# Kernel tuning notes

Measured on AMD Instinct MI355X. Metric: run time of the kernel, lower is better.

Reference implementation:

```python
import jax, jax.numpy as jnp
import numpy as np
import math

B, N, C, H = 8, 1024, 768, 12
D = C // H
HID = 4 * C
LS_INIT = 1e-6
LN_EPS = 1e-5


def setup_inputs() -> dict:
    key = jax.random.key(0)
    ks = jax.random.split(key, 8)
    s = lambda fan: 1.0 / math.sqrt(fan)
    return {
        'x': jax.random.normal(ks[0], (B, N, C), jnp.float32),
        'ln1_w': jnp.ones((C,), jnp.float32),
        'ln1_b': jnp.zeros((C,), jnp.float32),
        'qkv_w': jax.random.uniform(ks[1], (3 * C, C), jnp.float32, -s(C), s(C)),
        'qkv_b': jnp.zeros((3 * C,), jnp.float32),
        'proj_w': jax.random.uniform(ks[2], (C, C), jnp.float32, -s(C), s(C)),
        'proj_b': jnp.zeros((C,), jnp.float32),
        'attn_bias': jnp.asarray(-math.log(N), jnp.float32),
        'ls1': jnp.full((C,), LS_INIT, jnp.float32),
        'ln2_w': jnp.ones((C,), jnp.float32),
        'ln2_b': jnp.zeros((C,), jnp.float32),
        'w1': jax.random.uniform(ks[3], (HID, C), jnp.float32, -s(C), s(C)),
        'b1': jnp.zeros((HID,), jnp.float32),
        'w2': jax.random.uniform(ks[4], (C, HID), jnp.float32, -s(HID), s(HID)),
        'b2': jnp.zeros((C,), jnp.float32),
        'ls2': jnp.full((C,), LS_INIT, jnp.float32),
    }


def _layernorm(x, w, b):
    mu = jnp.mean(x, axis=-1, keepdims=True)
    var = jnp.mean(jnp.square(x - mu), axis=-1, keepdims=True)
    return (x - mu) * jax.lax.rsqrt(var + LN_EPS) * w + b


def reference(x, ln1_w, ln1_b, qkv_w, qkv_b, proj_w, proj_b, attn_bias,
              ls1, ln2_w, ln2_b, w1, b1, w2, b2, ls2):
    # --- sigmoid attention branch ---
    h = _layernorm(x, ln1_w, ln1_b)                       # [B,N,C]
    qkv = h @ qkv_w.T + qkv_b                              # [B,N,3C]
    qkv = qkv.reshape(B, N, 3, H, D).transpose(2, 0, 3, 1, 4)
    q, k, v = qkv[0], qkv[1], qkv[2]                       # [B,H,N,D]
    scale = D ** -0.5
    scores = jnp.einsum('bhnd,bhmd->bhnm', q, k) * scale + attn_bias
    attn = jax.nn.sigmoid(scores)                          # [B,H,N,N]
    o = jnp.einsum('bhnm,bhmd->bhnd', attn, v)             # [B,H,N,D]
    o = o.transpose(0, 2, 1, 3).reshape(B, N, C)
    o = o @ proj_w.T + proj_b
    x = x + o * ls1
    # --- MLP branch ---
    h2 = _layernorm(x, ln2_w, ln2_b)
    m = jax.nn.gelu(h2 @ w1.T + b1, approximate=False)
    m = m @ w2.T + b2
    x = x + m * ls2
    return x
```

## Files before the change

### kernel.cpp

```cpp
#include <hip/hip_runtime.h>
#include <math.h>

static constexpr int Bv   = 8;
static constexpr int Nv   = 1024;
static constexpr int Cv   = 768;
static constexpr int Hv   = 12;
static constexpr int HIDv = 3072;
static constexpr int Mv   = Bv * Nv;

typedef __attribute__((ext_vector_type(4)))  float f32x4;
typedef __attribute__((ext_vector_type(16))) float f32x16;
typedef __attribute__((ext_vector_type(8)))  short s16x8;
typedef __attribute__((ext_vector_type(4)))  short s16x4;

__device__ __forceinline__ short f2bf(float f) {
  union { float f; unsigned u; } c; c.f = f;
  unsigned r = c.u + 0x7fffu + ((c.u >> 16) & 1u);
  return (short)(r >> 16);
}

__device__ __forceinline__ void gload16(const void* g, void* l) {
  __builtin_amdgcn_global_load_lds(
      (const __attribute__((address_space(1))) unsigned*)g,
      (__attribute__((address_space(3))) unsigned*)l, 16, 0, 0);
}

__device__ __forceinline__ unsigned ldsaddr(const void* p) {
  return (unsigned)(size_t)(const __attribute__((address_space(3))) char*)p;
}

__device__ __forceinline__ float fsigmoid_exp2(float t) {
  return __builtin_amdgcn_rcpf(1.0f + __builtin_amdgcn_exp2f(t));
}

__global__ __launch_bounds__(256) void cvt_kernel(const float* __restrict__ in,
                                                  short* __restrict__ out, int n4) {
  int i = blockIdx.x * 256 + threadIdx.x;
  if (i >= n4) return;
  float4 v = ((const float4*)in)[i];
  short4 o;
  o.x = f2bf(v.x); o.y = f2bf(v.y); o.z = f2bf(v.z); o.w = f2bf(v.w);
  ((short4*)out)[i] = o;
}

__global__ __launch_bounds__(256) void ln_kernel(const float* __restrict__ x,
                                                 const float* __restrict__ w,
                                                 const float* __restrict__ b,
                                                 short* __restrict__ out) {
  const int wv = threadIdx.x >> 6, l = threadIdx.x & 63;
  const int row = blockIdx.x * 4 + wv;
  const float4* xr = (const float4*)(x + (size_t)row * Cv);
  float4 v[3];
  float s = 0.f, s2 = 0.f;
#pragma unroll
  for (int c = 0; c < 3; ++c) {
    v[c] = xr[c * 64 + l];
    s  += v[c].x + v[c].y + v[c].z + v[c].w;
    s2 += v[c].x * v[c].x + v[c].y * v[c].y + v[c].z * v[c].z + v[c].w * v[c].w;
  }
#pragma unroll
  for (int o = 32; o; o >>= 1) { s += __shfl_xor(s, o); s2 += __shfl_xor(s2, o); }
  const float mu  = s * (1.f / Cv);
  const float var = s2 * (1.f / Cv) - mu * mu;
  const float rs  = rsqrtf(var + 1e-5f);
  short4* orow = (short4*)(out + (size_t)row * Cv);
  const float4* wp = (const float4*)w;
  const float4* bp = (const float4*)b;
#pragma unroll
  for (int c = 0; c < 3; ++c) {
    float4 wv4 = wp[c * 64 + l], bv4 = bp[c * 64 + l];
    short4 o4;
    o4.x = f2bf((v[c].x - mu) * rs * wv4.x + bv4.x);
    o4.y = f2bf((v[c].y - mu) * rs * wv4.y + bv4.y);
    o4.z = f2bf((v[c].z - mu) * rs * wv4.z + bv4.z);
    o4.w = f2bf((v[c].w - mu) * rs * wv4.w + bv4.w);
    orow[c * 64 + l] = o4;
  }
}

template <int EPI>
__global__ __launch_bounds__(256) void gemm_bt(const short* __restrict__ A,
                                               const short* __restrict__ Bw,
                                               int Nn, int K,
                                               const float* __restrict__ bias,
                                               const float* __restrict__ ls,
                                               const float* __restrict__ resid,
                                               float* __restrict__ outF,
                                               short* __restrict__ outB) {
  __shared__ __align__(16) short ldsA[2][128 * 32];
  __shared__ __align__(16) short ldsB[2][128 * 32];
  const int tid = threadIdx.x, w = tid >> 6, l = tid & 63;
  const int nbx = Nn >> 7;
  const int bx = blockIdx.x % nbx, by = blockIdx.x / nbx;
  const int rowBase = by << 7, colBase = bx << 7;
  const int nK = K >> 5;
  const int wr = w >> 1, wc = w & 1;
  const int lrow = l >> 2, lcb = (l & 3) * 8;

  f32x4 acc[4][4] = {};

  auto stage = [&](int buf, int kt) {
    const short* abase = A  + (size_t)rowBase * K + kt * 32;
    const short* bbase = Bw + (size_t)colBase * K + kt * 32;
#pragma unroll
    for (int i = 0; i < 2; ++i) {
      int r = w * 2 + i;
      gload16(abase + (size_t)(r * 16 + lrow) * K + lcb, &ldsA[buf][r * 512]);
      gload16(bbase + (size_t)(r * 16 + lrow) * K + lcb, &ldsB[buf][r * 512]);
    }
  };

  stage(0, 0);
  __syncthreads();
  int cur = 0;
  for (int kt = 0; kt < nK; ++kt) {
    if (kt + 1 < nK) stage(cur ^ 1, kt + 1);
    s16x8 af[4], bfr[4];
#pragma unroll
    for (int i = 0; i < 4; ++i) {
      af[i]  = *(const s16x8*)&ldsA[cur][(wr * 64 + i * 16 + (l & 15)) * 32 + (l >> 4) * 8];
      bfr[i] = *(const s16x8*)&ldsB[cur][(wc * 64 + i * 16 + (l & 15)) * 32 + (l >> 4) * 8];
    }
#pragma unroll
    for (int i = 0; i < 4; ++i)
#pragma unroll
      for (int j = 0; j < 4; ++j)
        acc[i][j] = __builtin_amdgcn_mfma_f32_16x16x32_bf16(af[i], bfr[j], acc[i][j], 0, 0, 0);
    __syncthreads();
    cur ^= 1;
  }

#pragma unroll
  for (int i = 0; i < 4; ++i)
#pragma unroll
    for (int j = 0; j < 4; ++j) {
      const int col = colBase + wc * 64 + j * 16 + (l & 15);
#pragma unroll
      for (int r4 = 0; r4 < 4; ++r4) {
        const int row = rowBase + wr * 64 + i * 16 + (l >> 4) * 4 + r4;
        float v = acc[i][j][r4];
        if (EPI == 0) {
          v += bias[col];
          outB[(size_t)row * Nn + col] = f2bf(v);
        } else if (EPI == 1) {
          v = (v + bias[col]) * ls[col] + resid[(size_t)row * Nn + col];
          outF[(size_t)row * Nn + col] = v;
        } else if (EPI == 2) {
          v += bias[col];
          v = v * fsigmoid_exp2(v * -2.4554669f);
          outB[(size_t)row * Nn + col] = f2bf(v);
        } else {
          v = (v + bias[col]) * ls[col];
          outF[(size_t)row * Nn + col] += v;
        }
      }
    }
}

__global__ __launch_bounds__(256) void attn_kernel(const short* __restrict__ qkv,
                                                   const float* __restrict__ pbias,
                                                   short* __restrict__ o) {
  __shared__ __align__(16) short ldsK[2][64 * 64];
  __shared__ __align__(16) short ldsV[2][64 * 64];
  const int tid = threadIdx.x, w = tid >> 6, l = tid & 63;
  const int qt = blockIdx.x & 7, bh = blockIdx.x >> 3;
  const int b = bh / Hv, h = bh % Hv;
  const int q0 = qt * 128;
  const float c1 = -0.125f * 1.44269504f;
  const float c0 = -pbias[0] * 1.44269504f;
  const size_t rstr = 3 * Cv;
  const short* qb = qkv + (size_t)b * Nv * rstr + h * 64;
  const short* kb = qb + Cv;
  const short* vb = qb + 2 * Cv;

  s16x8 qf[4];
  {
    const short* qrow = qb + (size_t)(q0 + w * 32 + (l & 31)) * rstr + (l >> 5) * 8;
#pragma unroll
    for (int dc = 0; dc < 4; ++dc) qf[dc] = *(const s16x8*)(qrow + dc * 16);
  }

  auto stage = [&](int buf, int t) {
#pragma unroll
    for (int i = 0; i < 2; ++i) {
      int r = w * 2 + i;
      int kv = r * 8 + (l >> 3);
      gload16(kb + (size_t)(t * 64 + kv) * rstr + (((l & 7) ^ (kv & 7)) << 3),
              &ldsK[buf][r * 512]);
      int s   = r * 8 + (l >> 3);
      int kv2 = ((s >> 2) << 2) + ((l & 7) >> 1);
      int d2  = ((s & 3) << 4) + ((l & 1) << 3);
      gload16(vb + (size_t)(t * 64 + kv2) * rstr + d2, &ldsV[buf][r * 512]);
    }
  };

  stage(0, 0);
  __syncthreads();

  f32x16 oacc[2] = {};
  int cur = 0;
  for (int t = 0; t < 16; ++t) {
    if (t + 1 < 16) stage(cur ^ 1, t + 1);

    f32x16 sacc[2] = {};
#pragma unroll
    for (int kvh = 0; kvh < 2; ++kvh) {
      const int kv = kvh * 32 + (l & 31);
#pragma unroll
      for (int dc = 0; dc < 4; ++dc) {
        s16x8 kf = *(const s16x8*)&ldsK[cur][kv * 64 + (((dc * 2 + (l >> 5)) ^ (kv & 7)) << 3)];
        sacc[kvh] = __builtin_amdgcn_mfma_f32_32x32x16_bf16(kf, qf[dc], sacc[kvh], 0, 0, 0);
      }
    }

    unsigned pw[4][4];
#pragma unroll
    for (int kvh = 0; kvh < 2; ++kvh) {
      float p[16];
#pragma unroll
      for (int r = 0; r < 16; ++r)
        p[r] = fsigmoid_exp2(sacc[kvh][r] * c1 + c0);
#pragma unroll
      for (int half = 0; half < 2; ++half) {
        const int c = kvh * 2 + half, rb = half * 8;
        unsigned a, bq, cc, dq;
        asm("v_cvt_pk_bf16_f32 %0,%1,%2" : "=v"(a)  : "v"(p[rb + 0]), "v"(p[rb + 1]));
        asm("v_cvt_pk_bf16_f32 %0,%1,%2" : "=v"(bq) : "v"(p[rb + 4]), "v"(p[rb + 5]));
        asm("v_cvt_pk_bf16_f32 %0,%1,%2" : "=v"(cc) : "v"(p[rb + 2]), "v"(p[rb + 3]));
        asm("v_cvt_pk_bf16_f32 %0,%1,%2" : "=v"(dq) : "v"(p[rb + 6]), "v"(p[rb + 7]));
        asm("v_permlane32_swap_b32 %0,%1" : "+v"(a),  "+v"(bq));
        asm("v_permlane32_swap_b32 %0,%1" : "+v"(cc), "+v"(dq));
        pw[c][0] = a; pw[c][1] = cc; pw[c][2] = bq; pw[c][3] = dq;
      }
    }

    const unsigned vlds = ldsaddr(&ldsV[cur][0]);
#pragma unroll
    for (int dt = 0; dt < 2; ++dt) {
      s16x4 t1[4], t2[4];
#pragma unroll
      for (int c = 0; c < 4; ++c) {
        int s1 = c * 16 + ((l >> 5) << 3) + dt * 2 + ((l >> 4) & 1);
        unsigned ad = vlds + (unsigned)(s1 * 128 + (l & 15) * 8);
        asm volatile("ds_read_b64_tr_b16 %0, %1"            : "=v"(t1[c]) : "v"(ad));
        asm volatile("ds_read_b64_tr_b16 %0, %1 offset:512" : "=v"(t2[c]) : "v"(ad));
      }
      asm volatile("s_waitcnt lgkmcnt(0)" ::: "memory");
      __builtin_amdgcn_sched_barrier(0);
#pragma unroll
      for (int c = 0; c < 4; ++c) {
        union { s16x4 q[2]; s16x8 v; } va;
        va.q[0] = t1[c]; va.q[1] = t2[c];
        union { unsigned u[4]; s16x8 v; } pb;
        pb.u[0] = pw[c][0]; pb.u[1] = pw[c][1]; pb.u[2] = pw[c][2]; pb.u[3] = pw[c][3];
        oacc[dt] = __builtin_amdgcn_mfma_f32_32x32x16_bf16(va.v, pb.v, oacc[dt], 0, 0, 0);
      }
    }

    __syncthreads();
    cur ^= 1;
  }

  __syncthreads();
  short* obuf = (short*)ldsK + w * 2048;
  {
    const int q = l & 31, hs = (l >> 5) << 3;
#pragma unroll
    for (int dt = 0; dt < 2; ++dt)
#pragma unroll
      for (int rg = 0; rg < 4; ++rg) {
        unsigned w0, w1;
        asm("v_cvt_pk_bf16_f32 %0,%1,%2" : "=v"(w0) : "v"(oacc[dt][rg * 4 + 0]), "v"(oacc[dt][rg * 4 + 1]));
        asm("v_cvt_pk_bf16_f32 %0,%1,%2" : "=v"(w1) : "v"(oacc[dt][rg * 4 + 2]), "v"(oacc[dt][rg * 4 + 3]));
        int slot = (dt * 4 + rg) ^ (q & 7);
        *(unsigned long long*)((char*)obuf + q * 128 + slot * 16 + hs) =
            (unsigned long long)w0 | ((unsigned long long)w1 << 32);
      }
  }
  __syncthreads();
  {
    const int q = l >> 1;
    const short* rrow = obuf + q * 64;
    short* orow = o + (size_t)(b * Nv + q0 + w * 32 + q) * Cv + h * 64 + (l & 1) * 32;
#pragma unroll
    for (int i = 0; i < 4; ++i) {
      int slot = (l & 1) * 4 + i;
      s16x8 vv = *(const s16x8*)(rrow + ((slot ^ (q & 7)) << 3));
      *(s16x8*)(orow + i * 8) = vv;
    }
  }
}

extern "C" void kernel_launch(void* const* d_in, const int* in_sizes, int n_in,
                              void* d_out, int out_size, void* d_ws, size_t ws_size,
                              hipStream_t stream) {
  const float* x      = (const float*)d_in[0];
  const float* ln1_w  = (const float*)d_in[1];
  const float* ln1_b  = (const float*)d_in[2];
  const float* qkv_w  = (const float*)d_in[3];
  const float* qkv_b  = (const float*)d_in[4];
  const float* proj_w = (const float*)d_in[5];
  const float* proj_b = (const float*)d_in[6];
  const float* attn_b = (const float*)d_in[7];
  const float* ls1    = (const float*)d_in[8];
  const float* ln2_w  = (const float*)d_in[9];
  const float* ln2_b  = (const float*)d_in[10];
  const float* w1     = (const float*)d_in[11];
  const float* b1     = (const float*)d_in[12];
  const float* w2     = (const float*)d_in[13];
  const float* b2     = (const float*)d_in[14];
  const float* ls2    = (const float*)d_in[15];
  float* out = (float*)d_out;

  char* ws = (char*)d_ws;
  short* wqkvb = (short*)ws;  ws += (size_t)3 * Cv * Cv * 2;
  short* wprjb = (short*)ws;  ws += (size_t)Cv * Cv * 2;
  short* w1b   = (short*)ws;  ws += (size_t)HIDv * Cv * 2;
  short* w2b   = (short*)ws;  ws += (size_t)Cv * HIDv * 2;
  short* bufA  = (short*)ws;  ws += (size_t)Mv * Cv * 2;
  short* bufB  = (short*)ws;

  cvt_kernel<<<(3 * Cv * Cv / 4) / 256, 256, 0, stream>>>(qkv_w, wqkvb, 3 * Cv * Cv / 4);
  cvt_kernel<<<(Cv * Cv / 4) / 256, 256, 0, stream>>>(proj_w, wprjb, Cv * Cv / 4);
  cvt_kernel<<<(HIDv * Cv / 4) / 256, 256, 0, stream>>>(w1, w1b, HIDv * Cv / 4);
  cvt_kernel<<<(Cv * HIDv / 4) / 256, 256, 0, stream>>>(w2, w2b, Cv * HIDv / 4);

  ln_kernel<<<Mv / 4, 256, 0, stream>>>(x, ln1_w, ln1_b, bufA);
  gemm_bt<0><<<(Mv / 128) * (3 * Cv / 128), 256, 0, stream>>>(
      bufA, wqkvb, 3 * Cv, Cv, qkv_b, nullptr, nullptr, nullptr, bufB);
  attn_kernel<<<Bv * Hv * (Nv / 128), 256, 0, stream>>>(bufB, attn_b, bufA);
  gemm_bt<1><<<(Mv / 128) * (Cv / 128), 256, 0, stream>>>(
      bufA, wprjb, Cv, Cv, proj_b, ls1, x, out, nullptr);
  ln_kernel<<<Mv / 4, 256, 0, stream>>>(out, ln2_w, ln2_b, bufA);
  gemm_bt<2><<<(Mv / 128) * (HIDv / 128), 256, 0, stream>>>(
      bufA, w1b, HIDv, Cv, b1, nullptr, nullptr, nullptr, bufB);
  gemm_bt<3><<<(Mv / 128) * (Cv / 128), 256, 0, stream>>>(
      bufB, w2b, Cv, HIDv, b2, ls2, nullptr, out, nullptr);
}
```

Measured before the change: 404.2 us.

## Use 64-row tiles for narrow GEMMs, XCD-aware block remap, merge weight conversions

```diff
diff --git a/kernel.cpp b/kernel.cpp
--- a/kernel.cpp
+++ b/kernel.cpp
@@ -33,10 +33,20 @@
   return __builtin_amdgcn_rcpf(1.0f + __builtin_amdgcn_exp2f(t));
 }
 
-__global__ __launch_bounds__(256) void cvt_kernel(const float* __restrict__ in,
-                                                  short* __restrict__ out, int n4) {
-  int i = blockIdx.x * 256 + threadIdx.x;
-  if (i >= n4) return;
+__global__ __launch_bounds__(256) void cvt4_kernel(const float* __restrict__ w0,
+                                                   const float* __restrict__ w1,
+                                                   const float* __restrict__ w2,
+                                                   const float* __restrict__ w3,
+                                                   short* __restrict__ o0,
+                                                   short* __restrict__ o1,
+                                                   short* __restrict__ o2,
+                                                   short* __restrict__ o3) {
+  int bid = blockIdx.x;
+  const float* in; short* out; int i;
+  if (bid < 1728)      { in = w0; out = o0; i = bid * 256 + threadIdx.x; }
+  else if (bid < 2304) { in = w1; out = o1; i = (bid - 1728) * 256 + threadIdx.x; }
+  else if (bid < 4608) { in = w2; out = o2; i = (bid - 2304) * 256 + threadIdx.x; }
+  else                 { in = w3; out = o3; i = (bid - 4608) * 256 + threadIdx.x; }
   float4 v = ((const float4*)in)[i];
   short4 o;
   o.x = f2bf(v.x); o.y = f2bf(v.y); o.z = f2bf(v.z); o.w = f2bf(v.w);
@@ -83,15 +93,14 @@
                                                const short* __restrict__ Bw,
                                                int Nn, int K,
                                                const float* __restrict__ bias,
-                                               const float* __restrict__ ls,
-                                               const float* __restrict__ resid,
-                                               float* __restrict__ outF,
                                                short* __restrict__ outB) {
   __shared__ __align__(16) short ldsA[2][128 * 32];
   __shared__ __align__(16) short ldsB[2][128 * 32];
   const int tid = threadIdx.x, w = tid >> 6, l = tid & 63;
   const int nbx = Nn >> 7;
-  const int bx = blockIdx.x % nbx, by = blockIdx.x / nbx;
+  const int cpx = (int)gridDim.x >> 3;
+  const int wg = ((int)blockIdx.x & 7) * cpx + ((int)blockIdx.x >> 3);
+  const int bx = wg % nbx, by = wg / nbx;
   const int rowBase = by << 7, colBase = bx << 7;
   const int nK = K >> 5;
   const int wr = w >> 1, wc = w & 1;
@@ -135,22 +144,84 @@
 #pragma unroll
     for (int j = 0; j < 4; ++j) {
       const int col = colBase + wc * 64 + j * 16 + (l & 15);
+      const float bcol = bias[col];
 #pragma unroll
       for (int r4 = 0; r4 < 4; ++r4) {
         const int row = rowBase + wr * 64 + i * 16 + (l >> 4) * 4 + r4;
-        float v = acc[i][j][r4];
-        if (EPI == 0) {
-          v += bias[col];
-          outB[(size_t)row * Nn + col] = f2bf(v);
-        } else if (EPI == 1) {
-          v = (v + bias[col]) * ls[col] + resid[(size_t)row * Nn + col];
-          outF[(size_t)row * Nn + col] = v;
-        } else if (EPI == 2) {
-          v += bias[col];
-          v = v * fsigmoid_exp2(v * -2.4554669f);
-          outB[(size_t)row * Nn + col] = f2bf(v);
+        float v = acc[i][j][r4] + bcol;
+        if (EPI == 2) v = v * fsigmoid_exp2(v * -2.4554669f);
+        outB[(size_t)row * Nn + col] = f2bf(v);
+      }
+    }
+}
+
+template <int EPI>
+__global__ __launch_bounds__(256) void gemm_sm(const short* __restrict__ A,
+                                               const short* __restrict__ Bw,
+                                               int Nn, int K,
+                                               const float* __restrict__ bias,
+                                               const float* __restrict__ ls,
+                                               const float* __restrict__ resid,
+                                               float* __restrict__ outF) {
+  __shared__ __align__(16) short ldsA[2][64 * 32];
+  __shared__ __align__(16) short ldsB[2][128 * 32];
+  const int tid = threadIdx.x, w = tid >> 6, l = tid & 63;
+  const int nbx = Nn >> 7;
+  const int cpx = (int)gridDim.x >> 3;
+  const int wg = ((int)blockIdx.x & 7) * cpx + ((int)blockIdx.x >> 3);
+  const int bx = wg % nbx, by = wg / nbx;
+  const int rowBase = by << 6, colBase = bx << 7;
+  const int nK = K >> 5;
+  const int wr = w >> 1, wc = w & 1;
+  const int lrow = l >> 2, lcb = (l & 3) * 8;
+
+  f32x4 acc[2][4] = {};
+
+  auto stage = [&](int buf, int kt) {
+    const short* abase = A  + (size_t)rowBase * K + kt * 32;
+    const short* bbase = Bw + (size_t)colBase * K + kt * 32;
+    gload16(abase + (size_t)(w * 16 + lrow) * K + lcb, &ldsA[buf][w * 512]);
+#pragma unroll
+    for (int i = 0; i < 2; ++i) {
+      int r = w * 2 + i;
+      gload16(bbase + (size_t)(r * 16 + lrow) * K + lcb, &ldsB[buf][r * 512]);
+    }
+  };
+
+  stage(0, 0);
+  __syncthreads();
+  int cur = 0;
+  for (int kt = 0; kt < nK; ++kt) {
+    if (kt + 1 < nK) stage(cur ^ 1, kt + 1);
+    s16x8 af[2], bfr[4];
+#pragma unroll
+    for (int i = 0; i < 2; ++i)
+      af[i]  = *(const s16x8*)&ldsA[cur][(wr * 32 + i * 16 + (l & 15)) * 32 + (l >> 4) * 8];
+#pragma unroll
+    for (int j = 0; j < 4; ++j)
+      bfr[j] = *(const s16x8*)&ldsB[cur][(wc * 64 + j * 16 + (l & 15)) * 32 + (l >> 4) * 8];
+#pragma unroll
+    for (int i = 0; i < 2; ++i)
+#pragma unroll
+      for (int j = 0; j < 4; ++j)
+        acc[i][j] = __builtin_amdgcn_mfma_f32_16x16x32_bf16(af[i], bfr[j], acc[i][j], 0, 0, 0);
+    __syncthreads();
+    cur ^= 1;
+  }
+
+#pragma unroll
+  for (int i = 0; i < 2; ++i)
+#pragma unroll
+    for (int j = 0; j < 4; ++j) {
+      const int col = colBase + wc * 64 + j * 16 + (l & 15);
+      const float bcol = bias[col], lscol = ls[col];
+#pragma unroll
+      for (int r4 = 0; r4 < 4; ++r4) {
+        const int row = rowBase + wr * 32 + i * 16 + (l >> 4) * 4 + r4;
+        float v = (acc[i][j][r4] + bcol) * lscol;
+        if (EPI == 1) {
+          outF[(size_t)row * Nn + col] = v + resid[(size_t)row * Nn + col];
         } else {
-          v = (v + bias[col]) * ls[col];
           outF[(size_t)row * Nn + col] += v;
         }
       }
@@ -320,20 +391,18 @@
   short* bufA  = (short*)ws;  ws += (size_t)Mv * Cv * 2;
   short* bufB  = (short*)ws;
 
-  cvt_kernel<<<(3 * Cv * Cv / 4) / 256, 256, 0, stream>>>(qkv_w, wqkvb, 3 * Cv * Cv / 4);
-  cvt_kernel<<<(Cv * Cv / 4) / 256, 256, 0, stream>>>(proj_w, wprjb, Cv * Cv / 4);
-  cvt_kernel<<<(HIDv * Cv / 4) / 256, 256, 0, stream>>>(w1, w1b, HIDv * Cv / 4);
-  cvt_kernel<<<(Cv * HIDv / 4) / 256, 256, 0, stream>>>(w2, w2b, Cv * HIDv / 4);
+  cvt4_kernel<<<6912, 256, 0, stream>>>(qkv_w, proj_w, w1, w2,
+                                        wqkvb, wprjb, w1b, w2b);
 
   ln_kernel<<<Mv / 4, 256, 0, stream>>>(x, ln1_w, ln1_b, bufA);
   gemm_bt<0><<<(Mv / 128) * (3 * Cv / 128), 256, 0, stream>>>(
-      bufA, wqkvb, 3 * Cv, Cv, qkv_b, nullptr, nullptr, nullptr, bufB);
+      bufA, wqkvb, 3 * Cv, Cv, qkv_b, bufB);
   attn_kernel<<<Bv * Hv * (Nv / 128), 256, 0, stream>>>(bufB, attn_b, bufA);
-  gemm_bt<1><<<(Mv / 128) * (Cv / 128), 256, 0, stream>>>(
-      bufA, wprjb, Cv, Cv, proj_b, ls1, x, out, nullptr);
+  gemm_sm<1><<<(Mv / 64) * (Cv / 128), 256, 0, stream>>>(
+      bufA, wprjb, Cv, Cv, proj_b, ls1, x, out);
   ln_kernel<<<Mv / 4, 256, 0, stream>>>(out, ln2_w, ln2_b, bufA);
   gemm_bt<2><<<(Mv / 128) * (HIDv / 128), 256, 0, stream>>>(
-      bufA, w1b, HIDv, Cv, b1, nullptr, nullptr, nullptr, bufB);
-  gemm_bt<3><<<(Mv / 128) * (Cv / 128), 256, 0, stream>>>(
-      bufB, w2b, Cv, HIDv, b2, ls2, nullptr, out, nullptr);
-}
+      bufA, w1b, HIDv, Cv, b1, bufB);
+  gemm_sm<3><<<(Mv / 64) * (Cv / 128), 256, 0, stream>>>(
+      bufB, w2b, Cv, HIDv, b2, ls2, nullptr, out);
+}
```

New measurement: 375.9 us. 1.08x faster.
